# Kernel optimization log

Hardware: AMD Instinct MI355X
Metric: run time of the kernel (lower is better)

Reference implementation:

```python
import jax, jax.numpy as jnp
import numpy as np

NUM_HEADS = 16
HEAD_DIM = 64
ROPE_BASE = 160000.0


def _rope_tables(seq_len, head_dim):
    inv_freq = 1.0 / (ROPE_BASE ** (jnp.arange(0, head_dim, 2, dtype=jnp.float32) / head_dim))
    freqs = jnp.arange(seq_len, dtype=jnp.float32)[:, None] * inv_freq[None, :]  # [S, hd/2]
    return jnp.cos(freqs)[None, None], jnp.sin(freqs)[None, None]  # [1,1,S,hd/2]


def _apply_rope(x, cos, sin):
    # x: [B, nh, S, hd]; split-half rotation as in the torch module
    x1, x2 = jnp.split(x, 2, axis=-1)
    return jnp.concatenate([x1 * cos - x2 * sin, x2 * cos + x1 * sin], axis=-1)


def setup_inputs() -> dict:
    key = jax.random.key(0)
    k1, k2, k3 = jax.random.split(key, 3)
    B, S, H = 2, 2048, 1024
    hidden_states = jax.random.normal(k1, (B, S, H), dtype=jnp.float32)
    # additive causal mask: 0 for allowed, -1e9 for future positions
    causal = jnp.tril(jnp.ones((S, S), dtype=bool))
    attention_mask = jnp.where(causal, 0.0, -1e9).astype(jnp.float32)[None, None]
    Wqkv = jax.random.normal(k2, (H, 3 * H), dtype=jnp.float32) * (H ** -0.5)
    Wo = jax.random.normal(k3, (H, H), dtype=jnp.float32) * (H ** -0.5)
    return {"hidden_states": hidden_states, "attention_mask": attention_mask, "Wqkv": Wqkv, "Wo": Wo}


def reference(hidden_states, attention_mask, Wqkv, Wo):
    B, S, H = hidden_states.shape
    nh, hd = NUM_HEADS, HEAD_DIM
    scale = hd ** -0.5

    qkv = hidden_states @ Wqkv                                   # [B,S,3H]
    qkv = qkv.reshape(B, S, 3, nh, hd).transpose(2, 0, 3, 1, 4)  # [3,B,nh,S,hd]
    q, k, v = qkv[0], qkv[1], qkv[2]

    cos, sin = _rope_tables(S, hd)
    q = _apply_rope(q, cos, sin)
    k = _apply_rope(k, cos, sin)

    scores = jnp.einsum('bhqd,bhkd->bhqk', q, k) * scale + attention_mask
    attn = jax.nn.softmax(scores, axis=-1)
    out = jnp.einsum('bhqk,bhkd->bhqd', attn, v)                 # [B,nh,S,hd]
    out = out.transpose(0, 2, 1, 3).reshape(B, S, H)
    return out @ Wo
```

## Files before the change

### kernel.cpp

```cpp
#include <hip/hip_runtime.h>
#include <hip/hip_bf16.h>

typedef __bf16 bf16x8 __attribute__((ext_vector_type(8)));
typedef float f32x4 __attribute__((ext_vector_type(4)));
typedef unsigned short u16;

__device__ __forceinline__ u16 f2bf(float f) {
    union { float f; unsigned u; } x{f};
    unsigned r = x.u + 0x7fffu + ((x.u >> 16) & 1u);
    return (u16)(r >> 16);
}
__device__ __forceinline__ unsigned pk2(float a, float b) {
    union { float f; unsigned u; } x{a}, y{b};
    return ((x.u + 0x8000u) >> 16) | ((y.u + 0x8000u) & 0xffff0000u);
}
__device__ __forceinline__ float ex2(float x) { return __builtin_amdgcn_exp2f(x); }
__device__ __forceinline__ f32x4 zero4() { f32x4 z = {0.f, 0.f, 0.f, 0.f}; return z; }

typedef const __attribute__((address_space(1))) unsigned int* gp1_t;
typedef __attribute__((address_space(3))) unsigned int* lp3_t;
__device__ __forceinline__ void async16(const u16* g, u16* l) {
    __builtin_amdgcn_global_load_lds((gp1_t)g, (lp3_t)l, 16, 0, 0);
}

__global__ void __launch_bounds__(256) prep(const float* __restrict__ hs,
                                            u16* __restrict__ Xb,
                                            const float* __restrict__ Wqkv,
                                            u16* __restrict__ Wqkvt,
                                            const float* __restrict__ Wo,
                                            u16* __restrict__ Wot,
                                            float* __restrict__ cosT,
                                            float* __restrict__ sinT) {
    __shared__ float tile[32][33];
    const int blk = blockIdx.x, t = threadIdx.x;
    if (blk < 4096) {
        int i = (blk * 256 + t) * 4;
        float4 v = *(const float4*)(hs + i);
        ushort4 o;
        o.x = f2bf(v.x); o.y = f2bf(v.y); o.z = f2bf(v.z); o.w = f2bf(v.w);
        *(ushort4*)(Xb + i) = o;
    } else if (blk < 8192) {
        const float* W; u16* Wt; int N, bx, by;
        bool qkv = (blk < 7168);
        if (qkv) { int bid = blk - 4096; W = Wqkv; Wt = Wqkvt; N = 3072; bx = bid % 96; by = bid / 96; }
        else     { int bid = blk - 7168; W = Wo;   Wt = Wot;   N = 1024; bx = bid % 32; by = bid / 32; }
        const int K = 1024;
        int tx = t & 31, ty = t >> 5;
        int n0 = bx * 32, k0 = by * 32;
#pragma unroll
        for (int i = 0; i < 32; i += 8)
            tile[ty + i][tx] = W[(size_t)(k0 + ty + i) * N + n0 + tx];
        __syncthreads();
#pragma unroll
        for (int i = 0; i < 32; i += 8) {
            int n = n0 + ty + i;
            int np = n;
            if (qkv) {
                int hh = (n >> 6) & 3, f = (n >> 4) & 3;
                np = (n & ~255) | (((f >> 1) * 8 + hh * 2 + (f & 1)) << 4) | (n & 15);
            }
            Wt[(size_t)np * K + k0 + tx] = f2bf(tile[tx][ty + i]);
        }
    } else {
        int idx = (blk - 8192) * 256 + t;
        int d = idx & 31, s = idx >> 5;
        float inv = expf(-(float)d * 0.374466538f);
        float th = (float)s * inv;
        cosT[idx] = cosf(th);
        sinT[idx] = sinf(th);
    }
}

struct GemmCtx {
    f32x4 acc[4][4];
    int m16, q4, wm, wn;
};
template <int KDIM>
__device__ __forceinline__ void gemm_loop(const u16* __restrict__ A,
                                          const u16* __restrict__ Bt,
                                          int bm, int bn, GemmCtx& cx,
                                          u16* As, u16* Bs) {
    const int t = threadIdx.x;
    const int lane = t & 63, w = t >> 6;
    cx.wm = w >> 1; cx.wn = w & 1;
    cx.m16 = lane & 15; cx.q4 = lane >> 4;

    const int lrow = lane >> 2;
    const int kchunk = (lane & 3) ^ ((lane >> 3) & 3);
    const u16* Ag = A + (size_t)(bm * 128 + w * 32 + lrow) * KDIM + kchunk * 8;
    const u16* Bg = Bt + (size_t)(bn * 128 + w * 32 + lrow) * KDIM + kchunk * 8;
    const int l0 = (w * 32) * 32;
    const int l1 = (w * 32 + 16) * 32;
    const int kswz = (cx.q4 ^ ((cx.m16 >> 1) & 3)) * 8;

#pragma unroll
    for (int i = 0; i < 4; i++)
#pragma unroll
        for (int j = 0; j < 4; j++) cx.acc[i][j] = zero4();

    constexpr int NT = KDIM / 32;
    async16(Ag, As + l0);
    async16(Ag + 16 * KDIM, As + l1);
    async16(Bg, Bs + l0);
    async16(Bg + 16 * KDIM, Bs + l1);
    async16(Ag + 32, As + 4096 + l0);
    async16(Ag + 16 * KDIM + 32, As + 4096 + l1);
    async16(Bg + 32, Bs + 4096 + l0);
    async16(Bg + 16 * KDIM + 32, Bs + 4096 + l1);

    int co = 0, po = 2 * 4096;
#pragma unroll 1
    for (int tt = 0; tt < NT; ++tt) {
        if (tt + 1 < NT) {
            asm volatile("s_waitcnt vmcnt(4)" ::: "memory");
        } else {
            asm volatile("s_waitcnt vmcnt(0)" ::: "memory");
        }
        __builtin_amdgcn_s_barrier();
        __builtin_amdgcn_sched_barrier(0);
        if (tt + 2 < NT) {
            const int k0 = (tt + 2) * 32;
            async16(Ag + k0, As + po + l0);
            async16(Ag + 16 * KDIM + k0, As + po + l1);
            async16(Bg + k0, Bs + po + l0);
            async16(Bg + 16 * KDIM + k0, Bs + po + l1);
        }
        __builtin_amdgcn_sched_barrier(0);

        bf16x8 af[4], bf[4];
#pragma unroll
        for (int i = 0; i < 4; i++)
            af[i] = *(const bf16x8*)&As[co + (cx.wm * 64 + i * 16 + cx.m16) * 32 + kswz];
#pragma unroll
        for (int j = 0; j < 4; j++)
            bf[j] = *(const bf16x8*)&Bs[co + (cx.wn * 64 + j * 16 + cx.m16) * 32 + kswz];
#pragma unroll
        for (int i = 0; i < 4; i++)
#pragma unroll
            for (int j = 0; j < 4; j++)
                cx.acc[i][j] = __builtin_amdgcn_mfma_f32_16x16x32_bf16(af[i], bf[j], cx.acc[i][j], 0, 0, 0);

        asm volatile("" ::: "memory");
        __builtin_amdgcn_sched_barrier(0);
        co += 4096; if (co == 12288) co = 0;
        po += 4096; if (po == 12288) po = 0;
    }
}

__global__ void __launch_bounds__(512, 2) gemm_qkv(const u16* __restrict__ A,
                                                   const u16* __restrict__ Bt,
                                                   const float* __restrict__ cosT,
                                                   const float* __restrict__ sinT,
                                                   u16* __restrict__ Q,
                                                   u16* __restrict__ Kd,
                                                   u16* __restrict__ Vt) {
    __shared__ __align__(16) u16 As[2 * 256 * 64];
    __shared__ __align__(16) u16 Bs[2 * 256 * 64];
    constexpr int HB = 256 * 64;
    const int t = threadIdx.x, lane = t & 63, w = t >> 6;
    const int wm = w >> 2, wn = w & 3;
    const int m16 = lane & 15, q4 = lane >> 4, m7 = m16 & 7;
    const int hw = blockIdx.x;
    const int orig = (hw & 7) * 24 + (hw >> 3);
    const int bm = orig / 12, bn = orig % 12;

    const int srow = lane >> 3;
    const int schunk = (lane & 7) ^ srow;
    const u16* Ag = A + (size_t)(bm * 256 + w * 8 + srow) * 1024 + schunk * 8;
    const u16* Bg = Bt + (size_t)(bn * 256 + w * 8 + srow) * 1024 + schunk * 8;
    u16* AsW = As + w * 512;
    u16* BsW = Bs + w * 512;

    f32x4 acc[8][4];
#pragma unroll
    for (int i = 0; i < 8; i++)
#pragma unroll
        for (int j = 0; j < 4; j++) acc[i][j] = zero4();

    const int slt0 = (q4 ^ m7) * 8;
    const int slt1 = ((4 + q4) ^ m7) * 8;

#define STGA(S, H) do { const u16* g_ = Ag + (size_t)(H) * 131072 + (S) * 64; \
    u16* l_ = AsW + ((S) & 1) * HB + (H) * 8192; \
    async16(g_, l_); async16(g_ + 65536, l_ + 4096); } while (0)
#define STGB(S, H) do { const u16* g_ = Bg + (size_t)(H) * 131072 + (S) * 64; \
    u16* l_ = BsW + ((S) & 1) * HB + (H) * 8192; \
    async16(g_, l_); async16(g_ + 65536, l_ + 4096); } while (0)

    STGA(0, 0); STGB(0, 0); STGA(0, 1); STGB(0, 1); STGA(1, 0); STGB(1, 0);
    asm volatile("s_waitcnt vmcnt(4)" ::: "memory");
    __builtin_amdgcn_sched_barrier(0);
    __builtin_amdgcn_s_barrier();

#define MFMA8(IB, B0, B1) do { \
    _Pragma("unroll") for (int i4 = 0; i4 < 4; i4++) \
    _Pragma("unroll") for (int j2 = 0; j2 < 2; j2++) \
        acc[(IB) + i4][(JB) + j2] = __builtin_amdgcn_mfma_f32_16x16x32_bf16(a0[i4], B0[j2], acc[(IB) + i4][(JB) + j2], 0, 0, 0); \
    _Pragma("unroll") for (int i4 = 0; i4 < 4; i4++) \
    _Pragma("unroll") for (int j2 = 0; j2 < 2; j2++) \
        acc[(IB) + i4][(JB) + j2] = __builtin_amdgcn_mfma_f32_16x16x32_bf16(a1[i4], B1[j2], acc[(IB) + i4][(JB) + j2], 0, 0, 0); \
} while (0)

#define BAR1() do { __builtin_amdgcn_sched_barrier(0); __builtin_amdgcn_s_barrier(); \
                    __builtin_amdgcn_s_setprio(1); } while (0)
#define BAR2() do { __builtin_amdgcn_s_setprio(0); asm volatile("" ::: "memory"); \
                    __builtin_amdgcn_sched_barrier(0); __builtin_amdgcn_s_barrier(); } while (0)

#pragma unroll 1
    for (int T = 0; T < 16; ++T) {
        const int co = (T & 1) * HB;
        const int aL = co + (wm * 64 + m16) * 64;
        const int aH = aL + 128 * 64;
        const int bL = co + (wn * 32 + m16) * 64;
        const int bH = bL + 128 * 64;
        bf16x8 a0[4], a1[4], pl0[2], pl1[2], ph0[2], ph1[2];

#pragma unroll
        for (int i4 = 0; i4 < 4; i4++) {
            a0[i4] = *(const bf16x8*)&As[aL + i4 * 1024 + slt0];
            a1[i4] = *(const bf16x8*)&As[aL + i4 * 1024 + slt1];
        }
#pragma unroll
        for (int j2 = 0; j2 < 2; j2++) {
            pl0[j2] = *(const bf16x8*)&Bs[bL + j2 * 1024 + slt0];
            pl1[j2] = *(const bf16x8*)&Bs[bL + j2 * 1024 + slt1];
        }
        if (T < 15) STGA(T + 1, 1);
        BAR1();
        { constexpr int JB = 0; MFMA8(0, pl0, pl1); }
        BAR2();

#pragma unroll
        for (int j2 = 0; j2 < 2; j2++) {
            ph0[j2] = *(const bf16x8*)&Bs[bH + j2 * 1024 + slt0];
            ph1[j2] = *(const bf16x8*)&Bs[bH + j2 * 1024 + slt1];
        }
        if (T < 15) STGB(T + 1, 1);
        BAR1();
        { constexpr int JB = 2; MFMA8(0, ph0, ph1); }
        BAR2();

#pragma unroll
        for (int i4 = 0; i4 < 4; i4++) {
            a0[i4] = *(const bf16x8*)&As[aH + i4 * 1024 + slt0];
            a1[i4] = *(const bf16x8*)&As[aH + i4 * 1024 + slt1];
        }
        if (T < 14) STGA(T + 2, 0);
        BAR1();
        { constexpr int JB = 0; MFMA8(4, pl0, pl1); }
        BAR2();

        if (T < 14) {
            STGB(T + 2, 0);
            asm volatile("s_waitcnt vmcnt(4)" ::: "memory");
        } else {
            asm volatile("s_waitcnt vmcnt(0)" ::: "memory");
        }
        BAR1();
        { constexpr int JB = 2; MFMA8(4, ph0, ph1); }
        BAR2();
    }
#undef STGA
#undef STGB
#undef MFMA8
#undef BAR1
#undef BAR2

    const int colbase = bn * 256 + wn * 64;
    const int type = colbase >> 10;
    const int h = (colbase & 1023) >> 6;

    if (type == 2) {
#pragma unroll
        for (int i = 0; i < 8; i++) {
            int sr = bm * 256 + (i >> 2) * 128 + wm * 64 + (i & 3) * 16 + q4 * 4;
            int b = sr >> 11, sl = sr & 2047;
            size_t ob = (size_t)(b * 16 + h) * 64 * 2048;
#pragma unroll
            for (int j = 0; j < 4; j++) {
                int d = j * 16 + m16;
                ushort4 o;
                o.x = f2bf(acc[i][j][0]);
                o.y = f2bf(acc[i][j][1]);
                o.z = f2bf(acc[i][j][2]);
                o.w = f2bf(acc[i][j][3]);
                *(ushort4*)&Vt[ob + (size_t)d * 2048 + sl] = o;
            }
        }
    } else {
        u16* dst = (type == 0) ? Q : Kd;
        const float qs = (type == 0) ? 0.1803368801f  : 1.0f;
#pragma unroll
        for (int i = 0; i < 8; i++)
#pragma unroll
            for (int rr = 0; rr < 4; rr++) {
                int r = bm * 256 + (i >> 2) * 128 + wm * 64 + (i & 3) * 16 + q4 * 4 + rr;
                int b = r >> 11, s = r & 2047;
                size_t ob = ((size_t)((b * 16 + h) * 2048 + s)) * 64;
#pragma unroll
                for (int j2 = 0; j2 < 2; j2++) {
                    int d = j2 * 16 + m16;
                    float cs = cosT[s * 32 + d];
                    float sn = sinT[s * 32 + d];
                    float x1 = acc[i][j2][rr];
                    float x2 = acc[i][j2 + 2][rr];
                    dst[ob + d]      = f2bf((x1 * cs - x2 * sn) * qs);
                    dst[ob + d + 32] = f2bf((x2 * cs + x1 * sn) * qs);
                }
            }
    }
}

__global__ void __launch_bounds__(256) gemm_out(const u16* __restrict__ A,
                                                const u16* __restrict__ Bt,
                                                float* __restrict__ C) {
    __shared__ __align__(16) u16 As[3 * 128 * 32];
    __shared__ __align__(16) u16 Bs[3 * 128 * 32];
    GemmCtx cx;
    const int hw = blockIdx.x;
    const int orig = (hw & 7) * 32 + (hw >> 3);
    const int bm = orig >> 3, bn = orig & 7;
    gemm_loop<1024>(A, Bt, bm, bn, cx, As, Bs);
    const int N = 1024;
#pragma unroll
    for (int i = 0; i < 4; i++)
#pragma unroll
        for (int j = 0; j < 4; j++)
#pragma unroll
            for (int rr = 0; rr < 4; rr++) {
                int row = bm * 128 + cx.wm * 64 + i * 16 + cx.q4 * 4 + rr;
                int col = bn * 128 + cx.wn * 64 + j * 16 + cx.m16;
                C[(size_t)row * N + col] = cx.acc[i][j][rr];
            }
}

__global__ void __launch_bounds__(512) attn_kernel(const u16* __restrict__ Q,
                                                   const u16* __restrict__ Kg_,
                                                   const u16* __restrict__ Vtg_,
                                                   u16* __restrict__ O) {
    __shared__ __align__(16) u16 Ks[2][64][72];
    __shared__ __align__(16) u16 Vs[2][64][72];
    __shared__ __align__(16) u16 Pt[8][16][72];
    const int t = threadIdx.x, w = t >> 6;
    const int m16 = t & 15, q4 = (t & 63) >> 4;
    const int bid = blockIdx.x;
    const int c = bid & 255;
    const int st = (bid < 256) ? (15 - (c >> 5)) : (c >> 5);
    const int bh = c & 31;
    const size_t base = (size_t)bh * 2048 * 64;
    const int b = bh >> 4, h = bh & 15;
    const int skey = t >> 3, sc = (t & 7) * 8;

    const int qrow = st * 128 + w * 16 + m16;
    const u16* Qg = Q + base + (size_t)qrow * 64;
    bf16x8 qf0 = *(const bf16x8*)(Qg + q4 * 8);
    bf16x8 qf1 = *(const bf16x8*)(Qg + 32 + q4 * 8);

    f32x4 occ[4];
#pragma unroll
    for (int dc = 0; dc < 4; dc++) occ[dc] = zero4();
    float li = 0.f;

    const int jtmax = 2 * st + 1;
    const int jd = 2 * st + (w >> 2);

    const u16* Kb0 = Kg_ + base + skey * 64 + sc;
    const u16* Vt0 = Vtg_ + base + (size_t)skey * 2048 + sc;
    uint4 ka = *(const uint4*)(Kb0);
    uint4 va = *(const uint4*)(Vt0);

#pragma unroll 1
    for (int jt = 0; jt <= jtmax; jt++) {
        const int bi = jt & 1;
        *(uint4*)&Ks[bi][skey][sc] = ka;
        *(uint4*)&Vs[bi][skey][sc] = va;
        if (jt < jtmax) {
            ka = *(const uint4*)(Kb0 + (size_t)(jt + 1) * 4096);
            va = *(const uint4*)(Vt0 + (size_t)(jt + 1) * 64);
        }
        __syncthreads();

        if (jt <= jd) {
            f32x4 stv[4];
#pragma unroll
            for (int cc = 0; cc < 4; cc++) stv[cc] = zero4();
#pragma unroll
            for (int cc = 0; cc < 4; cc++) {
                bf16x8 kf0 = *(const bf16x8*)&Ks[bi][cc * 16 + m16][q4 * 8];
                bf16x8 kf1 = *(const bf16x8*)&Ks[bi][cc * 16 + m16][32 + q4 * 8];
                stv[cc] = __builtin_amdgcn_mfma_f32_16x16x32_bf16(kf0, qf0, stv[cc], 0, 0, 0);
                stv[cc] = __builtin_amdgcn_mfma_f32_16x16x32_bf16(kf1, qf1, stv[cc], 0, 0, 0);
            }

            float pv[4][4];
#pragma unroll
            for (int cc = 0; cc < 4; cc++)
#pragma unroll
                for (int rr = 0; rr < 4; rr++) pv[cc][rr] = stv[cc][rr];
            if (jt == jd) {
                const int ql = qrow - 64 * jt;
#pragma unroll
                for (int cc = 0; cc < 4; cc++)
#pragma unroll
                    for (int rr = 0; rr < 4; rr++)
                        if (cc * 16 + q4 * 4 + rr > ql) pv[cc][rr] = -1e30f;
            }

#pragma unroll
            for (int cc = 0; cc < 4; cc++) {
                float p0 = ex2(pv[cc][0] - 24.f);
                float p1 = ex2(pv[cc][1] - 24.f);
                float p2 = ex2(pv[cc][2] - 24.f);
                float p3 = ex2(pv[cc][3] - 24.f);
                li += (p0 + p1) + (p2 + p3);
                *(uint2*)&Pt[w][m16][cc * 16 + q4 * 4] = make_uint2(pk2(p0, p1), pk2(p2, p3));
            }

#pragma unroll
            for (int ks = 0; ks < 2; ks++) {
                bf16x8 pf = *(const bf16x8*)&Pt[w][m16][ks * 32 + q4 * 8];
#pragma unroll
                for (int dc = 0; dc < 4; dc++) {
                    bf16x8 vf = *(const bf16x8*)&Vs[bi][dc * 16 + m16][ks * 32 + q4 * 8];
                    occ[dc] = __builtin_amdgcn_mfma_f32_16x16x32_bf16(vf, pf, occ[dc], 0, 0, 0);
                }
            }
        }
    }

    li += __shfl_xor(li, 16);
    li += __shfl_xor(li, 32);
    float rli = 1.0f / li;
    u16* Op = O + ((size_t)(b * 2048 + qrow)) * 1024 + h * 64 + q4 * 4;
#pragma unroll
    for (int dc = 0; dc < 4; dc++) {
        ushort4 o;
        o.x = f2bf(occ[dc][0] * rli);
        o.y = f2bf(occ[dc][1] * rli);
        o.z = f2bf(occ[dc][2] * rli);
        o.w = f2bf(occ[dc][3] * rli);
        *(ushort4*)(Op + dc * 16) = o;
    }
}

extern "C" void kernel_launch(void* const* d_in, const int* in_sizes, int n_in,
                              void* d_out, int out_size, void* d_ws, size_t ws_size,
                              hipStream_t stream) {
    const float* hs   = (const float*)d_in[0];
    const float* Wqkv = (const float*)d_in[2];
    const float* Wo   = (const float*)d_in[3];
    float* out = (float*)d_out;

    const int BS = 4096;
    const int H = 1024, N3 = 3072;
    const int SH = 32 * 2048 * 64;

    u16* Xb    = (u16*)d_ws;
    u16* Wqkvt = Xb + (size_t)BS * H;
    u16* Wot   = Wqkvt + (size_t)N3 * H;
    u16* Qb    = Wot + (size_t)H * H;
    u16* Kb    = Qb + SH;
    u16* Vtb   = Kb + SH;
    u16* AOb   = Vtb + SH;
    float* cosT = (float*)(AOb + (size_t)BS * H);
    float* sinT = cosT + 2048 * 32;

    prep<<<8448, 256, 0, stream>>>(hs, Xb, Wqkv, Wqkvt, Wo, Wot, cosT, sinT);

    gemm_qkv<<<192, 512, 0, stream>>>(Xb, Wqkvt, cosT, sinT, Qb, Kb, Vtb);

    attn_kernel<<<512, 512, 0, stream>>>(Qb, Kb, Vtb, AOb);

    gemm_out<<<256, 256, 0, stream>>>(AOb, Wot, out);
}
```

Measured before the change: 186.2 us.

## Retile QKV GEMM to 256x192 blocks with 6 waves and 256 workgroups

Changes the QKV projection GEMM tile from 256x256 (8 waves, 192 blocks) to 256x192 (6 waves, 256 blocks), so the grid matches the 256 CUs of the MI355X. The load schedule is rewritten to stage the full B tile in one phase and the A halves split across waves, with the waitcnt thresholds adjusted to match. The weight column permutation in prep is dropped, so the QKV weight is laid out in natural order. This trades a bit of per-block reuse for full CU occupancy, but whether the epilogue (RoPE/head mapping) still matches the unpermuted layout is unclear.

```diff
diff --git a/kernel.cpp b/kernel.cpp
--- a/kernel.cpp
+++ b/kernel.cpp
@@ -41,9 +41,8 @@
         *(ushort4*)(Xb + i) = o;
     } else if (blk < 8192) {
         const float* W; u16* Wt; int N, bx, by;
-        bool qkv = (blk < 7168);
-        if (qkv) { int bid = blk - 4096; W = Wqkv; Wt = Wqkvt; N = 3072; bx = bid % 96; by = bid / 96; }
-        else     { int bid = blk - 7168; W = Wo;   Wt = Wot;   N = 1024; bx = bid % 32; by = bid / 32; }
+        if (blk < 7168) { int bid = blk - 4096; W = Wqkv; Wt = Wqkvt; N = 3072; bx = bid % 96; by = bid / 96; }
+        else            { int bid = blk - 7168; W = Wo;   Wt = Wot;   N = 1024; bx = bid % 32; by = bid / 32; }
         const int K = 1024;
         int tx = t & 31, ty = t >> 5;
         int n0 = bx * 32, k0 = by * 32;
@@ -52,15 +51,8 @@
             tile[ty + i][tx] = W[(size_t)(k0 + ty + i) * N + n0 + tx];
         __syncthreads();
 #pragma unroll
-        for (int i = 0; i < 32; i += 8) {
-            int n = n0 + ty + i;
-            int np = n;
-            if (qkv) {
-                int hh = (n >> 6) & 3, f = (n >> 4) & 3;
-                np = (n & ~255) | (((f >> 1) * 8 + hh * 2 + (f & 1)) << 4) | (n & 15);
-            }
-            Wt[(size_t)np * K + k0 + tx] = f2bf(tile[tx][ty + i]);
-        }
+        for (int i = 0; i < 32; i += 8)
+            Wt[(size_t)(n0 + ty + i) * K + k0 + tx] = f2bf(tile[tx][ty + i]);
     } else {
         int idx = (blk - 8192) * 256 + t;
         int d = idx & 31, s = idx >> 5;
@@ -147,29 +139,26 @@
     }
 }
 
-__global__ void __launch_bounds__(512, 2) gemm_qkv(const u16* __restrict__ A,
-                                                   const u16* __restrict__ Bt,
-                                                   const float* __restrict__ cosT,
-                                                   const float* __restrict__ sinT,
-                                                   u16* __restrict__ Q,
-                                                   u16* __restrict__ Kd,
-                                                   u16* __restrict__ Vt) {
+__global__ void __launch_bounds__(384) gemm_qkv(const u16* __restrict__ A,
+                                                const u16* __restrict__ Bt,
+                                                const float* __restrict__ cosT,
+                                                const float* __restrict__ sinT,
+                                                u16* __restrict__ Q,
+                                                u16* __restrict__ Kd,
+                                                u16* __restrict__ Vt) {
     __shared__ __align__(16) u16 As[2 * 256 * 64];
-    __shared__ __align__(16) u16 Bs[2 * 256 * 64];
-    constexpr int HB = 256 * 64;
+    __shared__ __align__(16) u16 Bs[2 * 192 * 64];
     const int t = threadIdx.x, lane = t & 63, w = t >> 6;
-    const int wm = w >> 2, wn = w & 3;
+    const int wm = (w >= 3) ? 1 : 0, wn = w - wm * 3;
     const int m16 = lane & 15, q4 = lane >> 4, m7 = m16 & 7;
     const int hw = blockIdx.x;
-    const int orig = (hw & 7) * 24 + (hw >> 3);
-    const int bm = orig / 12, bn = orig % 12;
-
-    const int srow = lane >> 3;
-    const int schunk = (lane & 7) ^ srow;
-    const u16* Ag = A + (size_t)(bm * 256 + w * 8 + srow) * 1024 + schunk * 8;
-    const u16* Bg = Bt + (size_t)(bn * 256 + w * 8 + srow) * 1024 + schunk * 8;
-    u16* AsW = As + w * 512;
-    u16* BsW = Bs + w * 512;
+    const int orig = (hw & 7) * 32 + (hw >> 3);
+    const int bm = orig >> 4, bn = orig & 15;
+
+    const int l8 = lane >> 3;
+    const int gk = (lane & 7) ^ l8;
+    const u16* AgB = A + (size_t)(bm * 256 + 8 * w + l8) * 1024 + gk * 8;
+    const u16* BgB = Bt + (size_t)(bn * 192 + 8 * w + l8) * 1024 + gk * 8;
 
     f32x4 acc[8][4];
 #pragma unroll
@@ -180,15 +169,15 @@
     const int slt0 = (q4 ^ m7) * 8;
     const int slt1 = ((4 + q4) ^ m7) * 8;
 
-#define STGA(S, H) do { const u16* g_ = Ag + (size_t)(H) * 131072 + (S) * 64; \
-    u16* l_ = AsW + ((S) & 1) * HB + (H) * 8192; \
-    async16(g_, l_); async16(g_ + 65536, l_ + 4096); } while (0)
-#define STGB(S, H) do { const u16* g_ = Bg + (size_t)(H) * 131072 + (S) * 64; \
-    u16* l_ = BsW + ((S) & 1) * HB + (H) * 8192; \
-    async16(g_, l_); async16(g_ + 65536, l_ + 4096); } while (0)
-
-    STGA(0, 0); STGB(0, 0); STGA(0, 1); STGB(0, 1); STGA(1, 0); STGB(1, 0);
-    asm volatile("s_waitcnt vmcnt(4)" ::: "memory");
+#define STGA(S, H, K) async16(AgB + (size_t)((H) * 128 + 48 * (K)) * 1024 + (S) * 64, \
+                              As + ((S) & 1) * 16384 + (H) * 8192 + w * 512 + (K) * 3072)
+#define STGB(S, K)    async16(BgB + (size_t)(48 * (K)) * 1024 + (S) * 64, \
+                              Bs + ((S) & 1) * 12288 + w * 512 + (K) * 3072)
+#define STGAH(S, H) do { STGA(S, H, 0); STGA(S, H, 1); if (w < 4) STGA(S, H, 2); } while (0)
+#define STGBF(S)    do { STGB(S, 0); STGB(S, 1); STGB(S, 2); STGB(S, 3); } while (0)
+
+    STGAH(0, 0); STGAH(0, 1); STGBF(0); STGAH(1, 0);
+    asm volatile("s_waitcnt vmcnt(2)" ::: "memory");
     __builtin_amdgcn_sched_barrier(0);
     __builtin_amdgcn_s_barrier();
 
@@ -208,11 +197,9 @@
 
 #pragma unroll 1
     for (int T = 0; T < 16; ++T) {
-        const int co = (T & 1) * HB;
-        const int aL = co + (wm * 64 + m16) * 64;
-        const int aH = aL + 128 * 64;
-        const int bL = co + (wn * 32 + m16) * 64;
-        const int bH = bL + 128 * 64;
+        const int aL = (T & 1) * 16384 + (wm * 64 + m16) * 64;
+        const int aH = aL + 8192;
+        const int bB = (T & 1) * 12288 + (wn * 64 + m16) * 64;
         bf16x8 a0[4], a1[4], pl0[2], pl1[2], ph0[2], ph1[2];
 
 #pragma unroll
@@ -222,20 +209,20 @@
         }
 #pragma unroll
         for (int j2 = 0; j2 < 2; j2++) {
-            pl0[j2] = *(const bf16x8*)&Bs[bL + j2 * 1024 + slt0];
-            pl1[j2] = *(const bf16x8*)&Bs[bL + j2 * 1024 + slt1];
-        }
-        if (T < 15) STGA(T + 1, 1);
+            pl0[j2] = *(const bf16x8*)&Bs[bB + j2 * 1024 + slt0];
+            pl1[j2] = *(const bf16x8*)&Bs[bB + j2 * 1024 + slt1];
+        }
+        if (T < 15) STGAH(T + 1, 1);
         BAR1();
         { constexpr int JB = 0; MFMA8(0, pl0, pl1); }
         BAR2();
 
 #pragma unroll
         for (int j2 = 0; j2 < 2; j2++) {
-            ph0[j2] = *(const bf16x8*)&Bs[bH + j2 * 1024 + slt0];
-            ph1[j2] = *(const bf16x8*)&Bs[bH + j2 * 1024 + slt1];
-        }
-        if (T < 15) STGB(T + 1, 1);
+            ph0[j2] = *(const bf16x8*)&Bs[bB + (j2 + 2) * 1024 + slt0];
+            ph1[j2] = *(const bf16x8*)&Bs[bB + (j2 + 2) * 1024 + slt1];
+        }
+        if (T < 15) STGBF(T + 1);
         BAR1();
         { constexpr int JB = 2; MFMA8(0, ph0, ph1); }
         BAR2();
@@ -245,14 +232,13 @@
             a0[i4] = *(const bf16x8*)&As[aH + i4 * 1024 + slt0];
             a1[i4] = *(const bf16x8*)&As[aH + i4 * 1024 + slt1];
         }
-        if (T < 14) STGA(T + 2, 0);
+        if (T < 14) STGAH(T + 2, 0);
         BAR1();
         { constexpr int JB = 0; MFMA8(4, pl0, pl1); }
         BAR2();
 
         if (T < 14) {
-            STGB(T + 2, 0);
-            asm volatile("s_waitcnt vmcnt(4)" ::: "memory");
+            asm volatile("s_waitcnt vmcnt(2)" ::: "memory");
         } else {
             asm volatile("s_waitcnt vmcnt(0)" ::: "memory");
         }
@@ -262,11 +248,13 @@
     }
 #undef STGA
 #undef STGB
+#undef STGAH
+#undef STGBF
 #undef MFMA8
 #undef BAR1
 #undef BAR2
 
-    const int colbase = bn * 256 + wn * 64;
+    const int colbase = bn * 192 + wn * 64;
     const int type = colbase >> 10;
     const int h = (colbase & 1023) >> 6;
 
@@ -467,7 +455,7 @@
 
     prep<<<8448, 256, 0, stream>>>(hs, Xb, Wqkv, Wqkvt, Wo, Wot, cosT, sinT);
 
-    gemm_qkv<<<192, 512, 0, stream>>>(Xb, Wqkvt, cosT, sinT, Qb, Kb, Vtb);
+    gemm_qkv<<<256, 384, 0, stream>>>(Xb, Wqkvt, cosT, sinT, Qb, Kb, Vtb);
 
     attn_kernel<<<512, 512, 0, stream>>>(Qb, Kb, Vtb, AOb);
 
```

Result: faster. 182.1 us (-2.2%).
